# Kernel optimization log

Hardware: AMD Instinct MI355X
Metric: run time of the kernel (lower is better)

Reference implementation:

```python
import jax, jax.numpy as jnp
import numpy as np

B, C, H, W = 4, 256, 64, 64
NH, NQ, HD, WS = 4, 16, 64, 3   # num_heads, num_queries, head_dim, attn_window_size
PD = NH * HD                    # proj_dim = 256


def setup_inputs() -> dict:
    key = jax.random.key(0)
    ks = jax.random.split(key, 6)
    s = 0.02
    return {
        "x": jax.random.normal(ks[0], (B, C, H, W), jnp.float32),
        "kv_w": jax.random.normal(ks[1], (2 * PD, C), jnp.float32) * s,
        "dot_w": jax.random.normal(ks[2], (NH, NQ, HD), jnp.float32) * s,
        "head_w": jax.random.normal(ks[3], (HD, PD), jnp.float32) * s,
        "head_b": jnp.zeros((HD,), jnp.float32),
        "q_w": jax.random.normal(ks[4], (C, NQ * HD), jnp.float32) * s,
        "q_b": jnp.zeros((C,), jnp.float32),
    }


def _unfold(x, ws):
    """Sliding ws x ws patches over last two dims (stride 1, same padding).
    x: (..., h, w) -> (..., h, w, ws*ws), flattened in (i*ws + j) order
    matching torch's unfold(2).unfold(3)."""
    pad = ws // 2
    padw = [(0, 0)] * (x.ndim - 2) + [(pad, pad), (pad, pad)]
    xp = jnp.pad(x, padw)
    h, w = x.shape[-2], x.shape[-1]
    return jnp.stack(
        [xp[..., i:i + h, j:j + w] for i in range(ws) for j in range(ws)],
        axis=-1,
    )


def reference(x, kv_w, dot_w, head_w, head_b, q_w, q_b):
    b, c, h, w = x.shape
    # kv 1x1 conv, then split into k, v (each proj_dim channels)
    kv = jnp.einsum('oc,bchw->bohw', kv_w, x)
    k, v = jnp.split(kv, 2, axis=1)
    # grouped 1x1 conv: per-head head_dim -> num_queries (NOTE: no scale; the
    # original defines self.scale but never applies it in forward)
    kh = k.reshape(b, NH, HD, h, w)
    attn = jnp.einsum('bndhw,nqd->bnqhw', kh, dot_w)
    # unfold overlapping 3x3 windows (L = ws^2 = 9)
    attn_p = _unfold(attn, WS)                        # (b, n, q, h, w, L)
    v_p = _unfold(v.reshape(b, NH, HD, h, w), WS)     # (b, n, d, h, w, L)
    attn_p = jax.nn.softmax(attn_p, axis=-1)
    # per-pixel weighted sum over the window, arranged as (b, q, n, d, h, w)
    out = jnp.einsum('bnqhwl,bndhwl->bqndhw', attn_p, v_p)
    out = out.reshape(b, NQ, PD, h, w)                # (n d) -> proj_dim channels
    # head_proj: 1x1 conv proj_dim -> head_dim (dropout=0)
    y = jnp.einsum('op,bqphw->bqohw', head_w, out) + head_b[None, None, :, None, None]
    # query_proj: 1x1 conv (k*head_dim) -> dim (dropout=0)
    y = y.reshape(b, NQ * HD, h, w)
    z = jnp.einsum('oc,bchw->bohw', q_w, y) + q_b[None, :, None, None]
    return z
```

## Files before the change

### kernel.cpp

```cpp
#include <hip/hip_runtime.h>
#include <hip/hip_bf16.h>
#include <cstdint>

typedef __hip_bfloat16 bf16;
using bf16x8 = __attribute__((ext_vector_type(8))) short;
using f32x4  = __attribute__((ext_vector_type(4))) float;

#define HW_T 4096
#define B_T  4

__device__ __forceinline__ void async_copy16(const bf16* g, bf16* l) {
    __builtin_amdgcn_global_load_lds(
        (const __attribute__((address_space(1))) void*)g,
        (__attribute__((address_space(3))) void*)l, 16, 0, 0);
}
__device__ __forceinline__ short f2bs(float f) {
    bf16 h = __float2bfloat16(f);
    return *reinterpret_cast<short*>(&h);
}
__device__ __forceinline__ float bs2f(short s) {
    unsigned int u = ((unsigned int)(unsigned short)s) << 16;
    float f;
    __builtin_memcpy(&f, &u, 4);
    return f;
}

__global__ __launch_bounds__(256) void fuse_all(
    const float* __restrict__ kv_w, const float* __restrict__ dot_w,
    const float* __restrict__ head_w, const float* __restrict__ q_w,
    bf16* __restrict__ W, bf16* __restrict__ qw_b)
{
    const int rb = blockIdx.x;
    if (rb < 384) {
        const int r = rb, c = threadIdx.x;
        float acc = 0.f;
        if (r < 64) {
            const int n = r >> 4, q = r & 15;
            #pragma unroll 8
            for (int d = 0; d < 64; ++d)
                acc += dot_w[(n * 16 + q) * 64 + d] * kv_w[(size_t)(n * 64 + d) * 256 + c];
        } else if (r < 320) {
            const int rr = r - 64, n = rr >> 6, dh = rr & 63;
            #pragma unroll 8
            for (int dd = 0; dd < 64; ++dd)
                acc += head_w[dh * 256 + n * 64 + dd] * kv_w[(size_t)(256 + n * 64 + dd) * 256 + c];
        }
        W[r * 256 + c] = __float2bfloat16(acc);
    } else {
        const int i = (rb - 384) * 256 + threadIdx.x;
        qw_b[i] = __float2bfloat16(q_w[i]);
    }
}

__global__ __launch_bounds__(256) void gemm_xw(
    const float* __restrict__ x, const bf16* __restrict__ W,
    bf16* __restrict__ AH)
{
    __shared__ __align__(16) bf16 As[2][4][64][8];
    __shared__ __align__(16) bf16 Bs[2][4][128][8];
    const int tid  = threadIdx.x;
    const int wave = tid >> 6, lane = tid & 63;
    const int m0 = blockIdx.x * 64;
    const int n0 = blockIdx.y * 128;
    const int b  = blockIdx.z;
    const float* xb = x + (size_t)b * 256 * HW_T;

    const int px = tid & 63, c8 = tid >> 6;
    const int fi = lane & 15, quad = lane >> 4;
    const int wn = wave * 32;

    f32x4 acc[4][2] = {};
    float xr[8];

    {
        const float* xp = xb + (size_t)(c8 * 8) * HW_T + m0 + px;
        #pragma unroll
        for (int j = 0; j < 8; ++j) xr[j] = xp[(size_t)j * HW_T];
        #pragma unroll
        for (int i = 0; i < 2; ++i) {
            const int slot = i * 256 + tid;
            const int r = slot & 127, q = slot >> 7;
            async_copy16(W + (size_t)(n0 + r) * 256 + q * 8,
                         &Bs[0][0][0][0] + (size_t)(i * 256 + wave * 64) * 8);
        }
        bf16x8 pk;
        #pragma unroll
        for (int j = 0; j < 8; ++j) pk[j] = f2bs(xr[j]);
        *(bf16x8*)&As[0][c8][px][0] = pk;
    }

    for (int it = 0; it < 8; ++it) {
        const int cur = it & 1;
        __syncthreads();
        if (it < 7) {
            const int k1 = (it + 1) * 32;
            const float* xp = xb + (size_t)(k1 + c8 * 8) * HW_T + m0 + px;
            #pragma unroll
            for (int j = 0; j < 8; ++j) xr[j] = xp[(size_t)j * HW_T];
            #pragma unroll
            for (int i = 0; i < 2; ++i) {
                const int slot = i * 256 + tid;
                const int r = slot & 127, q = slot >> 7;
                async_copy16(W + (size_t)(n0 + r) * 256 + k1 + q * 8,
                             &Bs[cur ^ 1][0][0][0] + (size_t)(i * 256 + wave * 64) * 8);
            }
        }
        bf16x8 af[4], bfr[2];
        #pragma unroll
        for (int i = 0; i < 4; ++i)
            af[i] = *(const bf16x8*)&As[cur][quad][i * 16 + fi][0];
        #pragma unroll
        for (int j = 0; j < 2; ++j)
            bfr[j] = *(const bf16x8*)&Bs[cur][quad][wn + j * 16 + fi][0];
        #pragma unroll
        for (int i = 0; i < 4; ++i)
            #pragma unroll
            for (int j = 0; j < 2; ++j)
                acc[i][j] = __builtin_amdgcn_mfma_f32_16x16x32_bf16(
                    af[i], bfr[j], acc[i][j], 0, 0, 0);
        if (it < 7) {
            bf16x8 pk;
            #pragma unroll
            for (int j = 0; j < 8; ++j) pk[j] = f2bs(xr[j]);
            *(bf16x8*)&As[cur ^ 1][c8][px][0] = pk;
        }
    }

    bf16* Cp = AH + (size_t)b * HW_T * 384;
    #pragma unroll
    for (int i = 0; i < 4; ++i) {
        const int p = m0 + i * 16 + quad * 4;
        #pragma unroll
        for (int r = 0; r < 4; ++r)
            #pragma unroll
            for (int j = 0; j < 2; ++j)
                Cp[(size_t)(p + r) * 384 + n0 + wn + j * 16 + fi] =
                    __float2bfloat16(acc[i][j][r]);
    }
}

#define YPAD 1032
#define ATTN_LDS (64 * YPAD * 2 + 8 * 9 * 64 * 4)

__global__ __launch_bounds__(512) void attn_qy(
    const bf16* __restrict__ AH, const float* __restrict__ head_b,
    const bf16* __restrict__ qw, const float* __restrict__ q_b,
    float* __restrict__ z)
{
    extern __shared__ __align__(16) char smem[];
    bf16*  yL = (bf16*)smem;
    float* Pm = (float*)(smem + 64 * YPAD * 2) + (threadIdx.x >> 6) * 9 * 64;

    const int tid  = threadIdx.x;
    const int wave = tid >> 6, lane = tid & 63;
    const int p0  = blockIdx.x * 64;
    const int b   = p0 >> 12;
    const int hw0 = p0 & 4095;
    const int h   = hw0 >> 6;
    const int fi = lane & 15, quad = lane >> 4;
    const ushort* AHu = (const ushort*)AH;

    float hb[4];
    #pragma unroll
    for (int dt = 0; dt < 4; ++dt) hb[dt] = head_b[dt * 16 + fi];

    for (int pi = 0; pi < 8; ++pi) {
        const int w = wave * 8 + pi;
        int off[9]; float okf[9];
        #pragma unroll
        for (int l = 0; l < 9; ++l) {
            const int i = l / 3, j = l % 3;
            const int hh = h + i - 1, ww = w + j - 1;
            const bool ok = ((unsigned)hh < 64u) && ((unsigned)ww < 64u);
            off[l] = ((b << 12) + (ok ? hh : h) * 64 + (ok ? ww : w)) * 384;
            okf[l] = ok ? 1.0f : 0.0f;
        }
        {
            float lg[9];
            #pragma unroll
            for (int l = 0; l < 9; ++l)
                lg[l] = bs2f((short)AHu[(size_t)off[l] + lane]) * okf[l];
            float m = lg[0];
            #pragma unroll
            for (int l = 1; l < 9; ++l) m = fmaxf(m, lg[l]);
            float e[9], s = 0.f;
            #pragma unroll
            for (int l = 0; l < 9; ++l) { e[l] = __expf(lg[l] - m); s += e[l]; }
            const float inv = 1.0f / s;
            #pragma unroll
            for (int l = 0; l < 9; ++l) Pm[l * 64 + lane] = e[l] * inv * okf[l];
        }
        __syncthreads();

        bf16x8 afr;
        #pragma unroll
        for (int j = 0; j < 8; ++j) {
            const int k = quad * 8 + j;
            afr[j] = f2bs(Pm[(k >> 2) * 64 + (k & 3) * 16 + fi]);
        }
        f32x4 acc[4];
        #pragma unroll
        for (int dt = 0; dt < 4; ++dt) {
            acc[dt][0] = hb[dt]; acc[dt][1] = hb[dt];
            acc[dt][2] = hb[dt]; acc[dt][3] = hb[dt];
        }
        #pragma unroll
        for (int dt = 0; dt < 4; ++dt) {
            bf16x8 bfr;
            #pragma unroll
            for (int j = 0; j < 8; ++j) {
                const int k = quad * 8 + j;
                bfr[j] = (short)AHu[(size_t)off[k >> 2] + 64 + (k & 3) * 64 + dt * 16 + fi];
            }
            acc[dt] = __builtin_amdgcn_mfma_f32_16x16x32_bf16(afr, bfr, acc[dt], 0, 0, 0);
        }
        #pragma unroll
        for (int n = 0; n < 4; ++n) {
            float pv[4];
            #pragma unroll
            for (int r = 0; r < 4; ++r) pv[r] = Pm[8 * 64 + n * 16 + quad * 4 + r];
            #pragma unroll
            for (int dt = 0; dt < 4; ++dt) {
                const float hval =
                    bs2f((short)AHu[(size_t)off[8] + 64 + n * 64 + dt * 16 + fi]);
                #pragma unroll
                for (int r = 0; r < 4; ++r) acc[dt][r] = fmaf(pv[r], hval, acc[dt][r]);
            }
        }
        #pragma unroll
        for (int dt = 0; dt < 4; ++dt)
            #pragma unroll
            for (int r = 0; r < 4; ++r)
                yL[(size_t)w * YPAD + (quad * 4 + r) * 64 + dt * 16 + fi] =
                    __float2bfloat16(acc[dt][r]);
    }
    __syncthreads();

    f32x4 zacc[2][4] = {};
    bf16x8 af[2], afn[2];
    #pragma unroll
    for (int i = 0; i < 2; ++i)
        af[i] = *(const bf16x8*)&qw[(size_t)(wave * 32 + i * 16 + fi) * 1024 + quad * 8];

    #pragma unroll 2
    for (int k0 = 0; k0 < 1024; k0 += 32) {
        if (k0 < 992) {
            #pragma unroll
            for (int i = 0; i < 2; ++i)
                afn[i] = *(const bf16x8*)&qw[(size_t)(wave * 32 + i * 16 + fi) * 1024
                                             + k0 + 32 + quad * 8];
        }
        bf16x8 bfr[4];
        #pragma unroll
        for (int j = 0; j < 4; ++j)
            bfr[j] = *(const bf16x8*)&yL[(size_t)(j * 16 + fi) * YPAD + k0 + quad * 8];
        #pragma unroll
        for (int i = 0; i < 2; ++i)
            #pragma unroll
            for (int j = 0; j < 4; ++j)
                zacc[i][j] = __builtin_amdgcn_mfma_f32_16x16x32_bf16(
                    af[i], bfr[j], zacc[i][j], 0, 0, 0);
        af[0] = afn[0]; af[1] = afn[1];
    }

    #pragma unroll
    for (int i = 0; i < 2; ++i) {
        const int row0 = wave * 32 + i * 16 + quad * 4;
        #pragma unroll
        for (int r = 0; r < 4; ++r) {
            const float bv = q_b[row0 + r];
            #pragma unroll
            for (int j = 0; j < 4; ++j)
                z[((size_t)(b * 256 + row0 + r)) * HW_T + hw0 + j * 16 + fi] =
                    zacc[i][j][r] + bv;
        }
    }
}

extern "C" void kernel_launch(void* const* d_in, const int* in_sizes, int n_in,
                              void* d_out, int out_size, void* d_ws, size_t ws_size,
                              hipStream_t stream) {
    (void)in_sizes; (void)n_in; (void)out_size; (void)ws_size;
    const float* x      = (const float*)d_in[0];
    const float* kv_w   = (const float*)d_in[1];
    const float* dot_w  = (const float*)d_in[2];
    const float* head_w = (const float*)d_in[3];
    const float* head_b = (const float*)d_in[4];
    const float* q_w    = (const float*)d_in[5];
    const float* q_b    = (const float*)d_in[6];
    float* z = (float*)d_out;

    char* ws    = (char*)d_ws;
    bf16*  AH   = (bf16*)ws;
    bf16*  W    = (bf16*)(ws + 12582912);
    bf16*  qw_b = (bf16*)(ws + 12779520);

    static bool attr_done = []() {
        hipFuncSetAttribute((const void*)attn_qy,
                            hipFuncAttributeMaxDynamicSharedMemorySize, ATTN_LDS);
        return true;
    }();
    (void)attr_done;

    fuse_all<<<dim3(1408), 256, 0, stream>>>(kv_w, dot_w, head_w, q_w, W, qw_b);

    gemm_xw<<<dim3(64, 3, B_T), 256, 0, stream>>>(x, W, AH);

    attn_qy<<<dim3(256), 512, ATTN_LDS, stream>>>(AH, head_b, qw_b, q_b, z);
}
```

Before: 128.4 us.

## Retile xW GEMM to full-N blocks, pre-swizzle q_w, drop a barrier

The x·W GEMM now gives each block 32 pixels and all 384 output channels. Each x element is read from global memory once instead of three times, at the cost of half as many pixels per block and a larger B tile in LDS. q_w is converted to bf16 in a k-blocked, MFMA-fragment-friendly layout so the query-projection loads are contiguous 16-byte reads, and the conversion kernel launches fewer blocks. A __syncthreads between writing and reading the per-wave softmax probabilities is removed; because Pm is per-wave this relies on wave-level ordering, which could be a correctness risk.

```diff
diff --git a/kernel.cpp b/kernel.cpp
--- a/kernel.cpp
+++ b/kernel.cpp
@@ -28,7 +28,7 @@
 __global__ __launch_bounds__(256) void fuse_all(
     const float* __restrict__ kv_w, const float* __restrict__ dot_w,
     const float* __restrict__ head_w, const float* __restrict__ q_w,
-    bf16* __restrict__ W, bf16* __restrict__ qw_b)
+    bf16* __restrict__ W, bf16* __restrict__ qwF)
 {
     const int rb = blockIdx.x;
     if (rb < 384) {
@@ -47,8 +47,13 @@
         }
         W[r * 256 + c] = __float2bfloat16(acc);
     } else {
-        const int i = (rb - 384) * 256 + threadIdx.x;
-        qw_b[i] = __float2bfloat16(q_w[i]);
+        const int t  = (rb - 384) * 256 + threadIdx.x;
+        const int ch = t & 255, kb = t >> 8;
+        const float* src = q_w + (size_t)ch * 1024 + kb * 8;
+        bf16x8 pk;
+        #pragma unroll
+        for (int j = 0; j < 8; ++j) pk[j] = f2bs(src[j]);
+        *(bf16x8*)&qwF[(size_t)t * 8] = pk;
     }
 }
 
@@ -56,37 +61,37 @@
     const float* __restrict__ x, const bf16* __restrict__ W,
     bf16* __restrict__ AH)
 {
-    __shared__ __align__(16) bf16 As[2][4][64][8];
-    __shared__ __align__(16) bf16 Bs[2][4][128][8];
+    __shared__ __align__(16) bf16 As[2][4][32][8];
+    __shared__ __align__(16) bf16 Bs[2][4][384][8];
     const int tid  = threadIdx.x;
     const int wave = tid >> 6, lane = tid & 63;
-    const int m0 = blockIdx.x * 64;
-    const int n0 = blockIdx.y * 128;
-    const int b  = blockIdx.z;
+    const int p0 = blockIdx.x * 32;
+    const int b  = blockIdx.y;
     const float* xb = x + (size_t)b * 256 * HW_T;
-
-    const int px = tid & 63, c8 = tid >> 6;
     const int fi = lane & 15, quad = lane >> 4;
-    const int wn = wave * 32;
-
-    f32x4 acc[4][2] = {};
+    const int wn0 = wave * 96;
+
+    const int apx = tid & 31, ac8 = (tid >> 5) & 3;
+    const bool aStage = tid < 128;
+
+    f32x4 acc[2][6] = {};
     float xr[8];
 
-    {
-        const float* xp = xb + (size_t)(c8 * 8) * HW_T + m0 + px;
+    #pragma unroll
+    for (int i = 0; i < 6; ++i) {
+        const int s = i * 256 + tid;
+        const int ch = s % 384, q = s / 384;
+        async_copy16(W + (size_t)ch * 256 + q * 8,
+                     &Bs[0][0][0][0] + (size_t)(i * 256 + wave * 64) * 8);
+    }
+    if (aStage) {
+        const float* xp = xb + (size_t)(ac8 * 8) * HW_T + p0 + apx;
         #pragma unroll
         for (int j = 0; j < 8; ++j) xr[j] = xp[(size_t)j * HW_T];
-        #pragma unroll
-        for (int i = 0; i < 2; ++i) {
-            const int slot = i * 256 + tid;
-            const int r = slot & 127, q = slot >> 7;
-            async_copy16(W + (size_t)(n0 + r) * 256 + q * 8,
-                         &Bs[0][0][0][0] + (size_t)(i * 256 + wave * 64) * 8);
-        }
         bf16x8 pk;
         #pragma unroll
         for (int j = 0; j < 8; ++j) pk[j] = f2bs(xr[j]);
-        *(bf16x8*)&As[0][c8][px][0] = pk;
+        *(bf16x8*)&As[0][ac8][apx][0] = pk;
     }
 
     for (int it = 0; it < 8; ++it) {
@@ -94,47 +99,49 @@
         __syncthreads();
         if (it < 7) {
             const int k1 = (it + 1) * 32;
-            const float* xp = xb + (size_t)(k1 + c8 * 8) * HW_T + m0 + px;
-            #pragma unroll
-            for (int j = 0; j < 8; ++j) xr[j] = xp[(size_t)j * HW_T];
-            #pragma unroll
-            for (int i = 0; i < 2; ++i) {
-                const int slot = i * 256 + tid;
-                const int r = slot & 127, q = slot >> 7;
-                async_copy16(W + (size_t)(n0 + r) * 256 + k1 + q * 8,
+            #pragma unroll
+            for (int i = 0; i < 6; ++i) {
+                const int s = i * 256 + tid;
+                const int ch = s % 384, q = s / 384;
+                async_copy16(W + (size_t)ch * 256 + k1 + q * 8,
                              &Bs[cur ^ 1][0][0][0] + (size_t)(i * 256 + wave * 64) * 8);
             }
-        }
-        bf16x8 af[4], bfr[2];
-        #pragma unroll
-        for (int i = 0; i < 4; ++i)
+            if (aStage) {
+                const float* xp = xb + (size_t)(k1 + ac8 * 8) * HW_T + p0 + apx;
+                #pragma unroll
+                for (int j = 0; j < 8; ++j) xr[j] = xp[(size_t)j * HW_T];
+            }
+        }
+        bf16x8 af[2], bfr[6];
+        #pragma unroll
+        for (int i = 0; i < 2; ++i)
             af[i] = *(const bf16x8*)&As[cur][quad][i * 16 + fi][0];
         #pragma unroll
-        for (int j = 0; j < 2; ++j)
-            bfr[j] = *(const bf16x8*)&Bs[cur][quad][wn + j * 16 + fi][0];
-        #pragma unroll
-        for (int i = 0; i < 4; ++i)
-            #pragma unroll
-            for (int j = 0; j < 2; ++j)
+        for (int j = 0; j < 6; ++j)
+            bfr[j] = *(const bf16x8*)&Bs[cur][quad][wn0 + j * 16 + fi][0];
+        #pragma unroll
+        for (int i = 0; i < 2; ++i)
+            #pragma unroll
+            for (int j = 0; j < 6; ++j)
                 acc[i][j] = __builtin_amdgcn_mfma_f32_16x16x32_bf16(
                     af[i], bfr[j], acc[i][j], 0, 0, 0);
-        if (it < 7) {
+        if (it < 7 && aStage) {
             bf16x8 pk;
             #pragma unroll
             for (int j = 0; j < 8; ++j) pk[j] = f2bs(xr[j]);
-            *(bf16x8*)&As[cur ^ 1][c8][px][0] = pk;
-        }
-    }
-
-    bf16* Cp = AH + (size_t)b * HW_T * 384;
-    #pragma unroll
-    for (int i = 0; i < 4; ++i) {
-        const int p = m0 + i * 16 + quad * 4;
+            *(bf16x8*)&As[cur ^ 1][ac8][apx][0] = pk;
+        }
+    }
+
+    bf16* Cp = AH + ((size_t)b * HW_T + p0) * 384;
+    #pragma unroll
+    for (int i = 0; i < 2; ++i) {
+        const int pl = i * 16 + quad * 4;
         #pragma unroll
         for (int r = 0; r < 4; ++r)
             #pragma unroll
-            for (int j = 0; j < 2; ++j)
-                Cp[(size_t)(p + r) * 384 + n0 + wn + j * 16 + fi] =
+            for (int j = 0; j < 6; ++j)
+                Cp[(size_t)(pl + r) * 384 + wn0 + j * 16 + fi] =
                     __float2bfloat16(acc[i][j][r]);
     }
 }
@@ -144,7 +151,7 @@
 
 __global__ __launch_bounds__(512) void attn_qy(
     const bf16* __restrict__ AH, const float* __restrict__ head_b,
-    const bf16* __restrict__ qw, const float* __restrict__ q_b,
+    const bf16* __restrict__ qwF, const float* __restrict__ q_b,
     float* __restrict__ z)
 {
     extern __shared__ __align__(16) char smem[];
@@ -190,7 +197,6 @@
             #pragma unroll
             for (int l = 0; l < 9; ++l) Pm[l * 64 + lane] = e[l] * inv * okf[l];
         }
-        __syncthreads();
 
         bf16x8 afr;
         #pragma unroll
@@ -240,15 +246,15 @@
     bf16x8 af[2], afn[2];
     #pragma unroll
     for (int i = 0; i < 2; ++i)
-        af[i] = *(const bf16x8*)&qw[(size_t)(wave * 32 + i * 16 + fi) * 1024 + quad * 8];
+        af[i] = *(const bf16x8*)&qwF[((size_t)quad * 256 + wave * 32 + i * 16 + fi) * 8];
 
     #pragma unroll 2
     for (int k0 = 0; k0 < 1024; k0 += 32) {
         if (k0 < 992) {
+            const size_t kb = (size_t)((k0 + 32) >> 3) + quad;
             #pragma unroll
             for (int i = 0; i < 2; ++i)
-                afn[i] = *(const bf16x8*)&qw[(size_t)(wave * 32 + i * 16 + fi) * 1024
-                                             + k0 + 32 + quad * 8];
+                afn[i] = *(const bf16x8*)&qwF[(kb * 256 + wave * 32 + i * 16 + fi) * 8];
         }
         bf16x8 bfr[4];
         #pragma unroll
@@ -290,10 +296,10 @@
     const float* q_b    = (const float*)d_in[6];
     float* z = (float*)d_out;
 
-    char* ws    = (char*)d_ws;
-    bf16*  AH   = (bf16*)ws;
-    bf16*  W    = (bf16*)(ws + 12582912);
-    bf16*  qw_b = (bf16*)(ws + 12779520);
+    char* ws   = (char*)d_ws;
+    bf16*  AH  = (bf16*)ws;
+    bf16*  W   = (bf16*)(ws + 12582912);
+    bf16*  qwF = (bf16*)(ws + 12779520);
 
     static bool attr_done = []() {
         hipFuncSetAttribute((const void*)attn_qy,
@@ -302,9 +308,9 @@
     }();
     (void)attr_done;
 
-    fuse_all<<<dim3(1408), 256, 0, stream>>>(kv_w, dot_w, head_w, q_w, W, qw_b);
-
-    gemm_xw<<<dim3(64, 3, B_T), 256, 0, stream>>>(x, W, AH);
-
-    attn_qy<<<dim3(256), 512, ATTN_LDS, stream>>>(AH, head_b, qw_b, q_b, z);
-}
+    fuse_all<<<dim3(512), 256, 0, stream>>>(kv_w, dot_w, head_w, q_w, W, qwF);
+
+    gemm_xw<<<dim3(128, B_T), 256, 0, stream>>>(x, W, AH);
+
+    attn_qy<<<dim3(256), 512, ATTN_LDS, stream>>>(AH, head_b, qwF, q_b, z);
+}
```

Result: slower. 131.8 us (+2.6%).
